# Kernel tuning notes

Hardware: AMD Instinct MI355X
Metric: run time of the kernel (lower is better)

## Reference

```python
import jax, jax.numpy as jnp
from jax import lax
import numpy as np

VOCAB, EMB = 50000, 300
HID, NCLS = 100, 20
BATCH, SEQ = 128, 512
P_DROP = 0.5


def setup_inputs() -> dict:
    key = jax.random.key(0)
    ks = jax.random.split(key, 8)
    s_e = 1.0 / np.sqrt(EMB)
    s_h = 1.0 / np.sqrt(HID)
    return {
        "inputs_batch": jax.random.randint(ks[0], (BATCH, SEQ), 0, VOCAB, dtype=jnp.int64)
        if jax.config.jax_enable_x64 else jax.random.randint(ks[0], (BATCH, SEQ), 0, VOCAB, dtype=jnp.int32),
        "emb_table": jax.random.normal(ks[1], (VOCAB, EMB), dtype=jnp.float32),
        # GRUCell params (torch layout): gates order [r, z, n]
        "w_ih": jax.random.uniform(ks[2], (3 * HID, EMB), jnp.float32, -s_h, s_h),
        "w_hh": jax.random.uniform(ks[3], (3 * HID, HID), jnp.float32, -s_h, s_h),
        "b_ih": jax.random.uniform(ks[4], (3 * HID,), jnp.float32, -s_h, s_h),
        "b_hh": jax.random.uniform(ks[5], (3 * HID,), jnp.float32, -s_h, s_h),
        "w_lin": jax.random.uniform(ks[6], (NCLS, HID), jnp.float32, -s_h, s_h),
        "b_lin": jax.random.uniform(ks[7], (NCLS,), jnp.float32, -s_h, s_h),
    }


def reference(inputs_batch, emb_table, w_ih, w_hh, b_ih, b_hh, w_lin, b_lin):
    B, S = inputs_batch.shape
    H = w_hh.shape[1]
    keep = 1.0 - P_DROP
    dk1, dk2 = jax.random.split(jax.random.key(42))

    z_embed = emb_table[inputs_batch]                       # [B, S, E]
    m1 = jax.random.bernoulli(dk1, keep, z_embed.shape)     # dropout1 mask
    z_embed = jnp.where(m1, z_embed / keep, 0.0)
    x_seq = jnp.swapaxes(z_embed, 0, 1)                     # [S, B, E]
    m2 = jax.random.bernoulli(dk2, keep, (S, B, H))         # per-step dropout2 masks

    def step(h, inp):
        x, m = inp
        gi = x @ w_ih.T + b_ih                              # [B, 3H]
        gh = h @ w_hh.T + b_hh
        i_r, i_z, i_n = jnp.split(gi, 3, axis=-1)
        h_r, h_z, h_n = jnp.split(gh, 3, axis=-1)
        r = jax.nn.sigmoid(i_r + h_r)
        zg = jax.nn.sigmoid(i_z + h_z)
        n = jnp.tanh(i_n + r * h_n)
        h_new = (1.0 - zg) * n + zg * h
        h_d = jnp.where(m, h_new / keep, 0.0)
        y = jax.nn.log_softmax(h_d @ w_lin.T + b_lin, axis=1)  # [B, C]
        return h_new, y

    h0 = jnp.zeros((B, H), dtype=x_seq.dtype)
    _, ys = lax.scan(step, h0, (x_seq, m2))                 # ys: [S, B, C]
    return jnp.transpose(ys, (1, 2, 0))                     # [B, C, S]
```

## Files before the change

### kernel.cpp

```cpp
#include <hip/hip_runtime.h>
#include <hip/hip_bf16.h>
#include <cstdint>

#define BATCH 128
#define SEQ   512
#define EMB   300
#define HID   100
#define G3    300
#define NCLS  20
#define NROWS (SEQ * BATCH)

#define M1_WORDS 614400
#define M2_WORDS 204800

typedef __attribute__((ext_vector_type(4))) float f32x4;
typedef __attribute__((ext_vector_type(8))) short s16x8;
typedef __fp16 h16x2 __attribute__((ext_vector_type(2)));

__host__ __device__ __forceinline__ void threefry2x32(uint32_t k0, uint32_t k1,
                                                      uint32_t x0, uint32_t x1,
                                                      uint32_t* o0, uint32_t* o1) {
  uint32_t ks2 = k0 ^ k1 ^ 0x1BD11BDAu;
  x0 += k0; x1 += k1;
#define TFR(r) { x0 += x1; x1 = (x1 << (r)) | (x1 >> (32 - (r))); x1 ^= x0; }
  TFR(13) TFR(15) TFR(26) TFR(6)  x0 += k1;  x1 += ks2 + 1u;
  TFR(17) TFR(29) TFR(16) TFR(24) x0 += ks2; x1 += k0 + 2u;
  TFR(13) TFR(15) TFR(26) TFR(6)  x0 += k0;  x1 += k1 + 3u;
  TFR(17) TFR(29) TFR(16) TFR(24) x0 += k1;  x1 += ks2 + 4u;
  TFR(13) TFR(15) TFR(26) TFR(6)  x0 += ks2; x1 += k0 + 5u;
#undef TFR
  *o0 = x0; *o1 = x1;
}

__device__ __forceinline__ uint32_t rand_bits32(uint32_t ka, uint32_t kb, uint32_t flat) {
  uint32_t a, b;
  threefry2x32(ka, kb, 0u, flat, &a, &b);
  return a ^ b;
}

__device__ __forceinline__ short f2bf(float f) {
  union { float f; uint32_t u; } c; c.f = f;
  uint32_t u = c.u;
  return (short)((u + 0x7FFFu + ((u >> 16) & 1u)) >> 16);
}

__device__ __forceinline__ void bar_lds() {
  __asm__ __volatile__("s_waitcnt lgkmcnt(0)" ::: "memory");
  __builtin_amdgcn_s_barrier();
  __asm__ __volatile__("" ::: "memory");
}

__device__ __forceinline__ float swz_xor4(float x) {
  return __builtin_bit_cast(float,
      __builtin_amdgcn_ds_swizzle(__builtin_bit_cast(int, x), 0x101F));
}

__global__ __launch_bounds__(256) void k_mask(uint32_t* __restrict__ M1w,
                                              uint32_t* __restrict__ M2w,
                                              uint32_t k1a, uint32_t k1b,
                                              uint32_t k2a, uint32_t k2b) {
  const int i = blockIdx.x * 256 + threadIdx.x;
  uint32_t ka, kb, base;
  uint32_t* dst;
  if (i < M1_WORDS) { ka = k1a; kb = k1b; base = (uint32_t)i * 32u; dst = M1w + i; }
  else { ka = k2a; kb = k2b; base = (uint32_t)(i - M1_WORDS) * 32u; dst = M2w + (i - M1_WORDS); }
  uint32_t w = 0u;
#pragma unroll
  for (int j = 0; j < 32; ++j) {
    uint32_t bits = rand_bits32(ka, kb, base + (uint32_t)j);
    w |= ((~bits) >> 31) << j;
  }
  *dst = w;
}

__global__ __launch_bounds__(256) void k_prepw(const float* __restrict__ w_ih,
                                               short* __restrict__ Wb) {
  int i8 = (blockIdx.x * 256 + threadIdx.x) * 8;
  if (i8 >= 304 * 320) return;
  short o[8];
#pragma unroll
  for (int j = 0; j < 8; ++j) {
    int pos = i8 + j;
    int n = pos / 320, k = pos - (pos / 320) * 320;
    float v = (n < 300 && k < 300) ? w_ih[(size_t)n * EMB + k] : 0.f;
    o[j] = f2bf(v);
  }
  *(s16x8*)(Wb + i8) = *(s16x8*)o;
}

__global__ __launch_bounds__(256) void k_prepx(const int* __restrict__ inputs,
                                               const float* __restrict__ emb,
                                               const uint32_t* __restrict__ M1w,
                                               short* __restrict__ Xb) {
  const int i8 = blockIdx.x * 256 + threadIdx.x;
  const int r = i8 / 40, c8 = i8 - r * 40;
  const int e = c8 * 8;
  const int b = r & 127, sq = r >> 7;
  short o[8];
  if (e >= 300) {
#pragma unroll
    for (int j = 0; j < 8; ++j) o[j] = 0;
  } else {
    const int tok = inputs[b * SEQ + sq];
    const float* er = emb + (size_t)tok * EMB + e;
    float xa[8];
    if (e + 8 <= 300) {
      float4 v0 = *(const float4*)(er);
      float4 v1 = *(const float4*)(er + 4);
      xa[0] = v0.x; xa[1] = v0.y; xa[2] = v0.z; xa[3] = v0.w;
      xa[4] = v1.x; xa[5] = v1.y; xa[6] = v1.z; xa[7] = v1.w;
    } else {
      float4 v0 = *(const float4*)(er);
      xa[0] = v0.x; xa[1] = v0.y; xa[2] = v0.z; xa[3] = v0.w;
      xa[4] = xa[5] = xa[6] = xa[7] = 0.f;
    }
    const uint32_t flat = (uint32_t)((b * SEQ + sq) * EMB + e);
    uint64_t mw = (uint64_t)M1w[flat >> 5] | ((uint64_t)M1w[(flat >> 5) + 1] << 32);
    uint32_t mb = (uint32_t)(mw >> (flat & 31));
#pragma unroll
    for (int j = 0; j < 8; ++j)
      o[j] = f2bf(((mb >> j) & 1u) ? xa[j] * 2.f : 0.f);
  }
  *(s16x8*)(Xb + (size_t)i8 * 8) = *(s16x8*)o;
}

__global__ __launch_bounds__(512) void k_gi8(const short* __restrict__ Xb,
                                             const short* __restrict__ Wb,
                                             const float* __restrict__ b_ih,
                                             float* __restrict__ GI) {
  __shared__ short As[128 * 40];
  __shared__ short Bs[304 * 40];
  const int t = threadIdx.x;
  const int s = blockIdx.x;
  const int lane = t & 63, wave = t >> 6;
  const int wr = wave & 1;
  const int wc = wave >> 1;
  const int ml = lane & 15, quad = lane >> 4;
  const int arow = t >> 2;
  const int akq = t & 3;

  const int nfr = (wc < 3) ? 5 : 4;
  f32x4 acc[4][5];
#pragma unroll
  for (int i = 0; i < 4; ++i)
#pragma unroll
    for (int j = 0; j < 5; ++j) acc[i][j] = (f32x4){0.f, 0.f, 0.f, 0.f};

  const short* xrow = Xb + ((size_t)(s * 128) + arow) * 320;

  for (int c = 0; c < 10; ++c) {
    s16x8 av = *(const s16x8*)(xrow + c * 32 + akq * 8);
    s16x8 bv0, bv1, bv2;
    {
      int i0 = t;
      bv0 = *(const s16x8*)(Wb + (size_t)(i0 >> 2) * 320 + c * 32 + (i0 & 3) * 8);
      int i1 = t + 512;
      bv1 = *(const s16x8*)(Wb + (size_t)(i1 >> 2) * 320 + c * 32 + (i1 & 3) * 8);
      if (t < 192) {
        int i2 = t + 1024;
        bv2 = *(const s16x8*)(Wb + (size_t)(i2 >> 2) * 320 + c * 32 + (i2 & 3) * 8);
      }
    }
    if (c > 0) __syncthreads();
    *(s16x8*)&As[arow * 40 + akq * 8] = av;
    {
      int i0 = t;       *(s16x8*)&Bs[(i0 >> 2) * 40 + (i0 & 3) * 8] = bv0;
      int i1 = t + 512; *(s16x8*)&Bs[(i1 >> 2) * 40 + (i1 & 3) * 8] = bv1;
      if (t < 192) { int i2 = t + 1024; *(s16x8*)&Bs[(i2 >> 2) * 40 + (i2 & 3) * 8] = bv2; }
    }
    __syncthreads();
    s16x8 af[4];
#pragma unroll
    for (int mt = 0; mt < 4; ++mt)
      af[mt] = *(const s16x8*)&As[(wr * 64 + mt * 16 + ml) * 40 + quad * 8];
#pragma unroll
    for (int j = 0; j < 5; ++j) {
      if (j < nfr) {
        int nt = wc + 4 * j;
        s16x8 bf = *(const s16x8*)&Bs[(nt * 16 + ml) * 40 + quad * 8];
#pragma unroll
        for (int mt = 0; mt < 4; ++mt)
          acc[mt][j] = __builtin_amdgcn_mfma_f32_16x16x32_bf16(af[mt], bf, acc[mt][j], 0, 0, 0);
      }
    }
  }

#pragma unroll
  for (int j = 0; j < 5; ++j) {
    if (j < nfr) {
      int n = (wc + 4 * j) * 16 + ml;
      if (n < 300) {
        float bias = b_ih[n];
#pragma unroll
        for (int mt = 0; mt < 4; ++mt) {
#pragma unroll
          for (int i = 0; i < 4; ++i) {
            int brow = wr * 64 + mt * 16 + quad * 4 + i;
            GI[(size_t)(s * BATCH + brow) * G3 + n] = acc[mt][j][i] + bias;
          }
        }
      }
    }
  }
}

__global__ __launch_bounds__(512) void k_gi7(const int* __restrict__ inputs,
                                             const float* __restrict__ emb,
                                             const short* __restrict__ Wb,
                                             const float* __restrict__ b_ih,
                                             const uint32_t* __restrict__ M1w,
                                             float* __restrict__ GI) {
  __shared__ short As[128 * 40];
  __shared__ short Bs[304 * 40];
  __shared__ int idxs[128];
  const int t = threadIdx.x;
  const int s = blockIdx.x;
  const int lane = t & 63, wave = t >> 6;
  const int wr = wave & 1;
  const int wc = wave >> 1;
  const int ml = lane & 15, quad = lane >> 4;
  const int arow = t >> 2;
  const int akq = t & 3;

  if (t < 128) idxs[t] = inputs[t * SEQ + s];
  __syncthreads();

  const int nfr = (wc < 3) ? 5 : 4;
  f32x4 acc[4][5];
#pragma unroll
  for (int i = 0; i < 4; ++i)
#pragma unroll
    for (int j = 0; j < 5; ++j) acc[i][j] = (f32x4){0.f, 0.f, 0.f, 0.f};

  const int myidx = idxs[arow];

  for (int c = 0; c < 10; ++c) {
    const int e0 = c * 32 + akq * 8;
    float xa[8];
#pragma unroll
    for (int j = 0; j < 8; ++j) xa[j] = 0.f;
    if (e0 + 7 < 300) {
#pragma unroll
      for (int q4 = 0; q4 < 2; ++q4) {
        float4 v = *(const float4*)(emb + (size_t)myidx * EMB + e0 + q4 * 4);
        xa[q4 * 4 + 0] = v.x; xa[q4 * 4 + 1] = v.y; xa[q4 * 4 + 2] = v.z; xa[q4 * 4 + 3] = v.w;
      }
    } else if (e0 < 300) {
#pragma unroll
      for (int j = 0; j < 8; ++j) {
        int e = e0 + j;
        if (e < 300) xa[j] = emb[(size_t)myidx * EMB + e];
      }
    }
    uint32_t mb = 0;
    if (e0 < 300) {
      uint32_t base = (uint32_t)((arow * SEQ + s) * EMB + e0);
      uint64_t mw = (uint64_t)M1w[base >> 5] | ((uint64_t)M1w[(base >> 5) + 1] << 32);
      mb = (uint32_t)(mw >> (base & 31));
    }
    short sa[8];
#pragma unroll
    for (int j = 0; j < 8; ++j)
      sa[j] = f2bf(((mb >> j) & 1u) ? xa[j] * 2.f : 0.f);
    s16x8 bv0, bv1, bv2;
    {
      int i0 = t;
      bv0 = *(const s16x8*)(Wb + (size_t)(i0 >> 2) * 320 + c * 32 + (i0 & 3) * 8);
      int i1 = t + 512;
      bv1 = *(const s16x8*)(Wb + (size_t)(i1 >> 2) * 320 + c * 32 + (i1 & 3) * 8);
      if (t < 192) {
        int i2 = t + 1024;
        bv2 = *(const s16x8*)(Wb + (size_t)(i2 >> 2) * 320 + c * 32 + (i2 & 3) * 8);
      }
    }
    if (c > 0) __syncthreads();
    *(s16x8*)&As[arow * 40 + akq * 8] = *(s16x8*)&sa[0];
    {
      int i0 = t;       *(s16x8*)&Bs[(i0 >> 2) * 40 + (i0 & 3) * 8] = bv0;
      int i1 = t + 512; *(s16x8*)&Bs[(i1 >> 2) * 40 + (i1 & 3) * 8] = bv1;
      if (t < 192) { int i2 = t + 1024; *(s16x8*)&Bs[(i2 >> 2) * 40 + (i2 & 3) * 8] = bv2; }
    }
    __syncthreads();
    s16x8 af[4];
#pragma unroll
    for (int mt = 0; mt < 4; ++mt)
      af[mt] = *(const s16x8*)&As[(wr * 64 + mt * 16 + ml) * 40 + quad * 8];
#pragma unroll
    for (int j = 0; j < 5; ++j) {
      if (j < nfr) {
        int nt = wc + 4 * j;
        s16x8 bf = *(const s16x8*)&Bs[(nt * 16 + ml) * 40 + quad * 8];
#pragma unroll
        for (int mt = 0; mt < 4; ++mt)
          acc[mt][j] = __builtin_amdgcn_mfma_f32_16x16x32_bf16(af[mt], bf, acc[mt][j], 0, 0, 0);
      }
    }
  }

#pragma unroll
  for (int j = 0; j < 5; ++j) {
    if (j < nfr) {
      int n = (wc + 4 * j) * 16 + ml;
      if (n < 300) {
        float bias = b_ih[n];
#pragma unroll
        for (int mt = 0; mt < 4; ++mt) {
#pragma unroll
          for (int i = 0; i < 4; ++i) {
            int brow = wr * 64 + mt * 16 + quad * 4 + i;
            GI[(size_t)(s * BATCH + brow) * G3 + n] = acc[mt][j][i] + bias;
          }
        }
      }
    }
  }
}

__global__ __launch_bounds__(512, 1) void k_rnn11(const float* __restrict__ GI,
                                                  const float* __restrict__ w_hh,
                                                  const float* __restrict__ b_hh,
                                                  const uint8_t* __restrict__ M2,
                                                  float* __restrict__ Hd) {
  __shared__ __align__(16) uint32_t hp_s[2][64];
  const int t = threadIdx.x, b = blockIdx.x;
  const int u = t >> 2, ks = t & 3;
  const bool act = (u < 100);
  const bool gate = act && (ks == 0);
  const int uc = act ? u : 99;
  const int kplo = (ks < 2) ? ks * 13 : 26 + (ks - 2) * 12;
  const int np = (ks < 2) ? 13 : 12;

  const float* rowR = w_hh + (size_t)uc * HID;
  const float* rowZ = w_hh + (size_t)(uc + 100) * HID;
  const float* rowN = w_hh + (size_t)(uc + 200) * HID;
  const h16x2 z2 = (h16x2){(__fp16)0.f, (__fp16)0.f};
  h16x2 wR[13], wZ[13], wN[13];
#pragma unroll
  for (int j = 0; j < 13; ++j) {
    if (j < np) {
      int o = 2 * (kplo + j);
      wR[j] = __builtin_amdgcn_cvt_pkrtz(rowR[o], rowR[o + 1]);
      wZ[j] = __builtin_amdgcn_cvt_pkrtz(rowZ[o], rowZ[o + 1]);
      wN[j] = __builtin_amdgcn_cvt_pkrtz(rowN[o], rowN[o + 1]);
    } else { wR[j] = z2; wZ[j] = z2; wN[j] = z2; }
  }

  float bR0 = 0.f, bZ0 = 0.f, bN0 = 0.f;
  float gcR = 0.f, gcZ = 0.f, gcN = 0.f;
  uint8_t mc = 0;
  if (gate) {
    bR0 = b_hh[u]; bZ0 = b_hh[100 + u]; bN0 = b_hh[200 + u];
    const float* g0 = GI + (size_t)b * G3;
    gcR = g0[u]; gcZ = g0[100 + u]; gcN = g0[200 + u];
    mc = M2[(uint32_t)(b * HID + u) >> 3];
  }
  const int p = u >> 1;
  const int sidx = (p < 13) ? 0 : (p < 26) ? 1 : (p < 38) ? 2 : 3;
  const int spos = p - ((sidx < 2) ? sidx * 13 : 26 + (sidx - 2) * 12);
  const int slot = sidx * 16 + spos;
  const bool writer = gate && !(u & 1);

  if (t < 128) ((uint32_t*)hp_s)[t] = 0u;
  float hprev = 0.f;
  __syncthreads();

#define QPX(x, c) __builtin_bit_cast(float, __builtin_amdgcn_mov_dpp( \
    __builtin_bit_cast(int, (x)), (c), 0xF, 0xF, true))
#define DOT1(J, W) { h16x2 hh = __builtin_bit_cast(h16x2, (W)); \
    sR = __builtin_amdgcn_fdot2(wR[J], hh, sR, false); \
    sZ = __builtin_amdgcn_fdot2(wZ[J], hh, sZ, false); \
    sN = __builtin_amdgcn_fdot2(wN[J], hh, sN, false); }

#pragma unroll 2
  for (int s = 0; s < SEQ; ++s) {
    float gnR = 0.f, gnZ = 0.f, gnN = 0.f;
    uint8_t mn = 0;
    if (gate) {
      int sn = (s + 1 < SEQ) ? s + 1 : s;
      const float* gp = GI + (size_t)(sn * BATCH + b) * G3;
      gnR = gp[u]; gnZ = gp[100 + u]; gnN = gp[200 + u];
      mn = M2[(uint32_t)((sn * BATCH + b) * HID + u) >> 3];
    }

    if (act) {
      float sR = bR0, sZ = bZ0, sN = bN0;
      const uint32_t* hb = &hp_s[s & 1][0] + (ks << 4);
      uint4 h0 = *(const uint4*)hb;
      uint4 h1 = *(const uint4*)(hb + 4);
      uint4 h2 = *(const uint4*)(hb + 8);
      uint32_t h3 = hb[12];
      DOT1(0, h0.x)  DOT1(1, h0.y)  DOT1(2, h0.z)  DOT1(3, h0.w)
      DOT1(4, h1.x)  DOT1(5, h1.y)  DOT1(6, h1.z)  DOT1(7, h1.w)
      DOT1(8, h2.x)  DOT1(9, h2.y)  DOT1(10, h2.z) DOT1(11, h2.w)
      DOT1(12, h3)
      sR += QPX(sR, 0xB1); sZ += QPX(sZ, 0xB1); sN += QPX(sN, 0xB1);
      sR += QPX(sR, 0x4E); sZ += QPX(sZ, 0x4E); sN += QPX(sN, 0x4E);
      if (gate) {
        float r = 1.f / (1.f + __expf(-(gcR + sR)));
        float z = 1.f / (1.f + __expf(-(gcZ + sZ)));
        float xn = gcN + r * sN;
        float e2 = __expf(2.f * fabsf(xn));
        float n = copysignf(1.f - 2.f / (e2 + 1.f), xn);
        float hnew = (1.f - z) * n + z * hprev;
        hprev = hnew;
        uint32_t fl = (uint32_t)((s * BATCH + b) * HID + u);
        float hd = ((mc >> (fl & 7)) & 1) ? hnew * 2.f : 0.f;
        Hd[(size_t)(b * SEQ + s) * HID + u] = hd;
        float hoth = swz_xor4(hnew);
        if (writer)
          hp_s[(s & 1) ^ 1][slot] =
              __builtin_bit_cast(uint32_t, __builtin_amdgcn_cvt_pkrtz(hnew, hoth));
      }
    }
    gcR = gnR; gcZ = gnZ; gcN = gnN; mc = mn;
    bar_lds();
  }
#undef DOT1
#undef QPX
}

__global__ __launch_bounds__(64) void k_out(const float* __restrict__ Hd,
                                            const float* __restrict__ w_lin,
                                            const float* __restrict__ b_lin,
                                            float* __restrict__ out) {
  __shared__ float Wl[NCLS * HID];
  __shared__ float bl[NCLS];
  const int t = threadIdx.x;
  for (int i = t; i < NCLS * HID; i += 64) Wl[i] = w_lin[i];
  if (t < NCLS) bl[t] = b_lin[t];
  __syncthreads();

  const int r0 = (blockIdx.x * 64 + t) * 4;
  float acc[4][NCLS];
#pragma unroll
  for (int r = 0; r < 4; ++r)
#pragma unroll
    for (int c = 0; c < NCLS; ++c) acc[r][c] = bl[c];

  for (int k = 0; k < HID; k += 4) {
    float4 h0 = *(const float4*)(Hd + (size_t)(r0 + 0) * HID + k);
    float4 h1 = *(const float4*)(Hd + (size_t)(r0 + 1) * HID + k);
    float4 h2 = *(const float4*)(Hd + (size_t)(r0 + 2) * HID + k);
    float4 h3 = *(const float4*)(Hd + (size_t)(r0 + 3) * HID + k);
#pragma unroll
    for (int c = 0; c < NCLS; ++c) {
      float4 w4 = *(const float4*)&Wl[c * HID + k];
      acc[0][c] += h0.x * w4.x + h0.y * w4.y + h0.z * w4.z + h0.w * w4.w;
      acc[1][c] += h1.x * w4.x + h1.y * w4.y + h1.z * w4.z + h1.w * w4.w;
      acc[2][c] += h2.x * w4.x + h2.y * w4.y + h2.z * w4.z + h2.w * w4.w;
      acc[3][c] += h3.x * w4.x + h3.y * w4.y + h3.z * w4.z + h3.w * w4.w;
    }
  }

  float lse[4];
#pragma unroll
  for (int r = 0; r < 4; ++r) {
    float mx = acc[r][0];
#pragma unroll
    for (int c = 1; c < NCLS; ++c) mx = fmaxf(mx, acc[r][c]);
    float se = 0.f;
#pragma unroll
    for (int c = 0; c < NCLS; ++c) se += __expf(acc[r][c] - mx);
    lse[r] = mx + __logf(se);
  }
  const int b = r0 >> 9, s0 = r0 & 511;
#pragma unroll
  for (int c = 0; c < NCLS; ++c) {
    float4 o = make_float4(acc[0][c] - lse[0], acc[1][c] - lse[1],
                           acc[2][c] - lse[2], acc[3][c] - lse[3]);
    *(float4*)(out + (size_t)(b * NCLS + c) * SEQ + s0) = o;
  }
}

extern "C" void kernel_launch(void* const* d_in, const int* in_sizes, int n_in,
                              void* d_out, int out_size, void* d_ws, size_t ws_size,
                              hipStream_t stream) {
  const int*   inputs = (const int*)d_in[0];
  const float* emb    = (const float*)d_in[1];
  const float* w_ih   = (const float*)d_in[2];
  const float* w_hh   = (const float*)d_in[3];
  const float* b_ih   = (const float*)d_in[4];
  const float* b_hh   = (const float*)d_in[5];
  const float* w_lin  = (const float*)d_in[6];
  const float* b_lin  = (const float*)d_in[7];
  float* out = (float*)d_out;

  float* GI = (float*)d_ws;
  float* Hd = GI + (size_t)NROWS * G3;
  uint8_t* M1 = (uint8_t*)(Hd + (size_t)NROWS * HID);
  uint8_t* M2 = M1 + (size_t)M1_WORDS * 4;
  short* Wb = (short*)(M2 + (size_t)M2_WORDS * 4);
  short* Xb = Wb + 304 * 320;
  const size_t need_xb = 150272000;

  uint32_t dk1a, dk1b, dk2a, dk2b;
  threefry2x32(0u, 42u, 0u, 0u, &dk1a, &dk1b);
  threefry2x32(0u, 42u, 0u, 1u, &dk2a, &dk2b);

  k_mask<<<(M1_WORDS + M2_WORDS) / 256, 256, 0, stream>>>(
      (uint32_t*)M1, (uint32_t*)M2, dk1a, dk1b, dk2a, dk2b);
  k_prepw<<<(304 * 320 / 8 + 255) / 256, 256, 0, stream>>>(w_ih, Wb);
  if (ws_size >= need_xb) {
    k_prepx<<<65536 * 40 / 256, 256, 0, stream>>>(inputs, emb,
                                                  (const uint32_t*)M1, Xb);
    k_gi8<<<512, 512, 0, stream>>>(Xb, Wb, b_ih, GI);
  } else {
    k_gi7<<<512, 512, 0, stream>>>(inputs, emb, Wb, b_ih, (const uint32_t*)M1, GI);
  }
  k_rnn11<<<BATCH, 512, 0, stream>>>(GI, w_hh, b_hh, M2, Hd);
  k_out<<<256, 64, 0, stream>>>(Hd, w_lin, b_lin, out);
}
```

Baseline: 559.4 us.

## Fuse all stages into one cooperative persistent kernel with grid syncs

Replaces the chain of mask, weight prep, input prep, GEMM, recurrence and output kernels with a single cooperative kernel of 256 blocks that separates the stages with grid-wide syncs. The embedding gather is fused into the GEMM A-tile load, so the bf16 Xb staging buffer is dropped. The output kernel now runs with one thread per row across the whole grid. The aim is to remove launch gaps and the round trip through Xb; in exchange, only 256 blocks do the GEMM and mask work, and the recurrence stage leaves half the blocks idle. If the cooperative launch fails, the old multi-kernel path runs instead.

```diff
diff --git a/kernel.cpp b/kernel.cpp
--- a/kernel.cpp
+++ b/kernel.cpp
@@ -1,6 +1,9 @@
 #include <hip/hip_runtime.h>
+#include <hip/hip_cooperative_groups.h>
 #include <hip/hip_bf16.h>
 #include <cstdint>
+
+namespace cg = cooperative_groups;
 
 #define BATCH 128
 #define SEQ   512
@@ -55,6 +58,297 @@
       __builtin_amdgcn_ds_swizzle(__builtin_bit_cast(int, x), 0x101F));
 }
 
+__global__ __launch_bounds__(512, 4) void k_all(
+    const int* __restrict__ inputs, const float* __restrict__ emb,
+    const float* __restrict__ w_ih, const float* __restrict__ w_hh,
+    const float* __restrict__ b_ih, const float* __restrict__ b_hh,
+    const float* __restrict__ w_lin, const float* __restrict__ b_lin,
+    float* __restrict__ out, float* __restrict__ GI, float* __restrict__ Hd,
+    uint32_t* __restrict__ M1w, uint32_t* __restrict__ M2w,
+    short* __restrict__ Wb,
+    uint32_t k1a, uint32_t k1b, uint32_t k2a, uint32_t k2b) {
+  __shared__ __align__(16) char smem[35072];
+  const int t = threadIdx.x, bid = blockIdx.x;
+  const int flat = bid * 512 + t;
+
+  for (int i = flat; i < M1_WORDS + M2_WORDS; i += 256 * 512) {
+    uint32_t ka, kb, base;
+    uint32_t* dst;
+    if (i < M1_WORDS) { ka = k1a; kb = k1b; base = (uint32_t)i * 32u; dst = M1w + i; }
+    else { ka = k2a; kb = k2b; base = (uint32_t)(i - M1_WORDS) * 32u; dst = M2w + (i - M1_WORDS); }
+    uint32_t w = 0u;
+#pragma unroll
+    for (int j = 0; j < 32; ++j) {
+      uint32_t bits = rand_bits32(ka, kb, base + (uint32_t)j);
+      w |= ((~bits) >> 31) << j;
+    }
+    *dst = w;
+  }
+  if (flat < 304 * 320 / 8) {
+    const int i8 = flat * 8;
+    short o[8];
+#pragma unroll
+    for (int j = 0; j < 8; ++j) {
+      int pos = i8 + j;
+      int n = pos / 320, k = pos - (pos / 320) * 320;
+      float v = (n < 300 && k < 300) ? w_ih[(size_t)n * EMB + k] : 0.f;
+      o[j] = f2bf(v);
+    }
+    *(s16x8*)(Wb + i8) = *(s16x8*)o;
+  }
+  __threadfence();
+  cg::this_grid().sync();
+  __threadfence();
+
+  {
+    short* As = (short*)smem;
+    short* Bs = As + 128 * 40;
+    int* idxs = (int*)(Bs + 304 * 40);
+    const int lane = t & 63, wave = t >> 6;
+    const int wr = wave & 1, wc = wave >> 1;
+    const int ml = lane & 15, quad = lane >> 4;
+    const int arow = t >> 2, akq = t & 3;
+    const int nfr = (wc < 3) ? 5 : 4;
+
+    for (int si = 0; si < 2; ++si) {
+      const int s = bid * 2 + si;
+      __syncthreads();
+      if (t < 128) idxs[t] = inputs[t * SEQ + s];
+      __syncthreads();
+
+      f32x4 acc[4][5];
+#pragma unroll
+      for (int i = 0; i < 4; ++i)
+#pragma unroll
+        for (int j = 0; j < 5; ++j) acc[i][j] = (f32x4){0.f, 0.f, 0.f, 0.f};
+
+      const int myidx = idxs[arow];
+
+      for (int c = 0; c < 10; ++c) {
+        const int e0 = c * 32 + akq * 8;
+        float xa[8];
+#pragma unroll
+        for (int j = 0; j < 8; ++j) xa[j] = 0.f;
+        if (e0 + 7 < 300) {
+#pragma unroll
+          for (int q4 = 0; q4 < 2; ++q4) {
+            float4 v = *(const float4*)(emb + (size_t)myidx * EMB + e0 + q4 * 4);
+            xa[q4 * 4 + 0] = v.x; xa[q4 * 4 + 1] = v.y;
+            xa[q4 * 4 + 2] = v.z; xa[q4 * 4 + 3] = v.w;
+          }
+        } else if (e0 < 300) {
+#pragma unroll
+          for (int j = 0; j < 8; ++j) {
+            int e = e0 + j;
+            if (e < 300) xa[j] = emb[(size_t)myidx * EMB + e];
+          }
+        }
+        uint32_t mb = 0;
+        if (e0 < 300) {
+          uint32_t base = (uint32_t)((arow * SEQ + s) * EMB + e0);
+          uint64_t mw = (uint64_t)M1w[base >> 5] | ((uint64_t)M1w[(base >> 5) + 1] << 32);
+          mb = (uint32_t)(mw >> (base & 31));
+        }
+        short sa[8];
+#pragma unroll
+        for (int j = 0; j < 8; ++j)
+          sa[j] = f2bf(((mb >> j) & 1u) ? xa[j] * 2.f : 0.f);
+        s16x8 bv0, bv1, bv2;
+        {
+          int i0 = t;
+          bv0 = *(const s16x8*)(Wb + (size_t)(i0 >> 2) * 320 + c * 32 + (i0 & 3) * 8);
+          int i1 = t + 512;
+          bv1 = *(const s16x8*)(Wb + (size_t)(i1 >> 2) * 320 + c * 32 + (i1 & 3) * 8);
+          if (t < 192) {
+            int i2 = t + 1024;
+            bv2 = *(const s16x8*)(Wb + (size_t)(i2 >> 2) * 320 + c * 32 + (i2 & 3) * 8);
+          }
+        }
+        if (c > 0) __syncthreads();
+        *(s16x8*)&As[arow * 40 + akq * 8] = *(s16x8*)&sa[0];
+        {
+          int i0 = t;       *(s16x8*)&Bs[(i0 >> 2) * 40 + (i0 & 3) * 8] = bv0;
+          int i1 = t + 512; *(s16x8*)&Bs[(i1 >> 2) * 40 + (i1 & 3) * 8] = bv1;
+          if (t < 192) { int i2 = t + 1024; *(s16x8*)&Bs[(i2 >> 2) * 40 + (i2 & 3) * 8] = bv2; }
+        }
+        __syncthreads();
+        s16x8 af[4];
+#pragma unroll
+        for (int mt = 0; mt < 4; ++mt)
+          af[mt] = *(const s16x8*)&As[(wr * 64 + mt * 16 + ml) * 40 + quad * 8];
+#pragma unroll
+        for (int j = 0; j < 5; ++j) {
+          if (j < nfr) {
+            int nt = wc + 4 * j;
+            s16x8 bf = *(const s16x8*)&Bs[(nt * 16 + ml) * 40 + quad * 8];
+#pragma unroll
+            for (int mt = 0; mt < 4; ++mt)
+              acc[mt][j] = __builtin_amdgcn_mfma_f32_16x16x32_bf16(af[mt], bf, acc[mt][j], 0, 0, 0);
+          }
+        }
+      }
+
+#pragma unroll
+      for (int j = 0; j < 5; ++j) {
+        if (j < nfr) {
+          int n = (wc + 4 * j) * 16 + ml;
+          if (n < 300) {
+            float bias = b_ih[n];
+#pragma unroll
+            for (int mt = 0; mt < 4; ++mt) {
+#pragma unroll
+              for (int i = 0; i < 4; ++i) {
+                int brow = wr * 64 + mt * 16 + quad * 4 + i;
+                GI[(size_t)(s * BATCH + brow) * G3 + n] = acc[mt][j][i] + bias;
+              }
+            }
+          }
+        }
+      }
+    }
+  }
+  __threadfence();
+  cg::this_grid().sync();
+  __threadfence();
+
+  if (bid < BATCH) {
+    uint32_t (*hp_s)[64] = (uint32_t (*)[64])smem;
+    const int b = bid;
+    const int u = t >> 2, ks = t & 3;
+    const bool act = (u < 100);
+    const bool gate = act && (ks == 0);
+    const int uc = act ? u : 99;
+    const int kplo = (ks < 2) ? ks * 13 : 26 + (ks - 2) * 12;
+    const int np = (ks < 2) ? 13 : 12;
+
+    const float* rowR = w_hh + (size_t)uc * HID;
+    const float* rowZ = w_hh + (size_t)(uc + 100) * HID;
+    const float* rowN = w_hh + (size_t)(uc + 200) * HID;
+    const h16x2 z2 = (h16x2){(__fp16)0.f, (__fp16)0.f};
+    h16x2 wR[13], wZ[13], wN[13];
+#pragma unroll
+    for (int j = 0; j < 13; ++j) {
+      if (j < np) {
+        int o = 2 * (kplo + j);
+        wR[j] = __builtin_amdgcn_cvt_pkrtz(rowR[o], rowR[o + 1]);
+        wZ[j] = __builtin_amdgcn_cvt_pkrtz(rowZ[o], rowZ[o + 1]);
+        wN[j] = __builtin_amdgcn_cvt_pkrtz(rowN[o], rowN[o + 1]);
+      } else { wR[j] = z2; wZ[j] = z2; wN[j] = z2; }
+    }
+
+    float bR0 = 0.f, bZ0 = 0.f, bN0 = 0.f;
+    float gcR = 0.f, gcZ = 0.f, gcN = 0.f;
+    uint8_t mc = 0;
+    const uint8_t* M2 = (const uint8_t*)M2w;
+    if (gate) {
+      bR0 = b_hh[u]; bZ0 = b_hh[100 + u]; bN0 = b_hh[200 + u];
+      const float* g0 = GI + (size_t)b * G3;
+      gcR = g0[u]; gcZ = g0[100 + u]; gcN = g0[200 + u];
+      mc = M2[(uint32_t)(b * HID + u) >> 3];
+    }
+    const int p = u >> 1;
+    const int sidx = (p < 13) ? 0 : (p < 26) ? 1 : (p < 38) ? 2 : 3;
+    const int spos = p - ((sidx < 2) ? sidx * 13 : 26 + (sidx - 2) * 12);
+    const int slot = sidx * 16 + spos;
+    const bool writer = gate && !(u & 1);
+
+    if (t < 128) ((uint32_t*)hp_s)[t] = 0u;
+    float hprev = 0.f;
+    __syncthreads();
+
+#define QPX(x, c) __builtin_bit_cast(float, __builtin_amdgcn_mov_dpp( \
+    __builtin_bit_cast(int, (x)), (c), 0xF, 0xF, true))
+#define DOT1(J, W) { h16x2 hh = __builtin_bit_cast(h16x2, (W)); \
+    sR = __builtin_amdgcn_fdot2(wR[J], hh, sR, false); \
+    sZ = __builtin_amdgcn_fdot2(wZ[J], hh, sZ, false); \
+    sN = __builtin_amdgcn_fdot2(wN[J], hh, sN, false); }
+
+#pragma unroll 2
+    for (int s = 0; s < SEQ; ++s) {
+      float gnR = 0.f, gnZ = 0.f, gnN = 0.f;
+      uint8_t mn = 0;
+      if (gate) {
+        int sn = (s + 1 < SEQ) ? s + 1 : s;
+        const float* gp = GI + (size_t)(sn * BATCH + b) * G3;
+        gnR = gp[u]; gnZ = gp[100 + u]; gnN = gp[200 + u];
+        mn = M2[(uint32_t)((sn * BATCH + b) * HID + u) >> 3];
+      }
+
+      if (act) {
+        float sR = bR0, sZ = bZ0, sN = bN0;
+        const uint32_t* hb = &hp_s[s & 1][0] + (ks << 4);
+        uint4 h0 = *(const uint4*)hb;
+        uint4 h1 = *(const uint4*)(hb + 4);
+        uint4 h2 = *(const uint4*)(hb + 8);
+        uint32_t h3 = hb[12];
+        DOT1(0, h0.x)  DOT1(1, h0.y)  DOT1(2, h0.z)  DOT1(3, h0.w)
+        DOT1(4, h1.x)  DOT1(5, h1.y)  DOT1(6, h1.z)  DOT1(7, h1.w)
+        DOT1(8, h2.x)  DOT1(9, h2.y)  DOT1(10, h2.z) DOT1(11, h2.w)
+        DOT1(12, h3)
+        sR += QPX(sR, 0xB1); sZ += QPX(sZ, 0xB1); sN += QPX(sN, 0xB1);
+        sR += QPX(sR, 0x4E); sZ += QPX(sZ, 0x4E); sN += QPX(sN, 0x4E);
+        if (gate) {
+          float r = 1.f / (1.f + __expf(-(gcR + sR)));
+          float z = 1.f / (1.f + __expf(-(gcZ + sZ)));
+          float xn = gcN + r * sN;
+          float e2 = __expf(2.f * fabsf(xn));
+          float n = copysignf(1.f - 2.f / (e2 + 1.f), xn);
+          float hnew = (1.f - z) * n + z * hprev;
+          hprev = hnew;
+          uint32_t fl = (uint32_t)((s * BATCH + b) * HID + u);
+          float hd = ((mc >> (fl & 7)) & 1) ? hnew * 2.f : 0.f;
+          Hd[(size_t)(b * SEQ + s) * HID + u] = hd;
+          float hoth = swz_xor4(hnew);
+          if (writer)
+            hp_s[(s & 1) ^ 1][slot] =
+                __builtin_bit_cast(uint32_t, __builtin_amdgcn_cvt_pkrtz(hnew, hoth));
+        }
+      }
+      gcR = gnR; gcZ = gnZ; gcN = gnN; mc = mn;
+      bar_lds();
+    }
+#undef DOT1
+#undef QPX
+  }
+  __threadfence();
+  cg::this_grid().sync();
+  __threadfence();
+
+  {
+    float* Wl = (float*)smem;
+    float* bl = Wl + NCLS * HID;
+    __syncthreads();
+    for (int i = t; i < NCLS * HID; i += 512) Wl[i] = w_lin[i];
+    if (t < NCLS) bl[t] = b_lin[t];
+    __syncthreads();
+    if (flat < NROWS) {
+      const int r = flat, b = r >> 9, s0 = r & 511;
+      const float* hrow = Hd + (size_t)r * HID;
+      float acc[NCLS];
+#pragma unroll
+      for (int c = 0; c < NCLS; ++c) acc[c] = bl[c];
+      for (int k = 0; k < HID; k += 4) {
+        const float4 h = *(const float4*)(hrow + k);
+#pragma unroll
+        for (int c = 0; c < NCLS; ++c) {
+          const float4 w4 = *(const float4*)&Wl[c * HID + k];
+          acc[c] += h.x * w4.x + h.y * w4.y + h.z * w4.z + h.w * w4.w;
+        }
+      }
+      float mx = acc[0];
+#pragma unroll
+      for (int c = 1; c < NCLS; ++c) mx = fmaxf(mx, acc[c]);
+      float se = 0.f;
+#pragma unroll
+      for (int c = 0; c < NCLS; ++c) se += __expf(acc[c] - mx);
+      const float lse = mx + __logf(se);
+#pragma unroll
+      for (int c = 0; c < NCLS; ++c)
+        out[(size_t)(b * NCLS + c) * SEQ + s0] = acc[c] - lse;
+    }
+  }
+}
+
 __global__ __launch_bounds__(256) void k_mask(uint32_t* __restrict__ M1w,
                                               uint32_t* __restrict__ M2w,
                                               uint32_t k1a, uint32_t k1b,
@@ -86,122 +380,6 @@
     o[j] = f2bf(v);
   }
   *(s16x8*)(Wb + i8) = *(s16x8*)o;
-}
-
-__global__ __launch_bounds__(256) void k_prepx(const int* __restrict__ inputs,
-                                               const float* __restrict__ emb,
-                                               const uint32_t* __restrict__ M1w,
-                                               short* __restrict__ Xb) {
-  const int i8 = blockIdx.x * 256 + threadIdx.x;
-  const int r = i8 / 40, c8 = i8 - r * 40;
-  const int e = c8 * 8;
-  const int b = r & 127, sq = r >> 7;
-  short o[8];
-  if (e >= 300) {
-#pragma unroll
-    for (int j = 0; j < 8; ++j) o[j] = 0;
-  } else {
-    const int tok = inputs[b * SEQ + sq];
-    const float* er = emb + (size_t)tok * EMB + e;
-    float xa[8];
-    if (e + 8 <= 300) {
-      float4 v0 = *(const float4*)(er);
-      float4 v1 = *(const float4*)(er + 4);
-      xa[0] = v0.x; xa[1] = v0.y; xa[2] = v0.z; xa[3] = v0.w;
-      xa[4] = v1.x; xa[5] = v1.y; xa[6] = v1.z; xa[7] = v1.w;
-    } else {
-      float4 v0 = *(const float4*)(er);
-      xa[0] = v0.x; xa[1] = v0.y; xa[2] = v0.z; xa[3] = v0.w;
-      xa[4] = xa[5] = xa[6] = xa[7] = 0.f;
-    }
-    const uint32_t flat = (uint32_t)((b * SEQ + sq) * EMB + e);
-    uint64_t mw = (uint64_t)M1w[flat >> 5] | ((uint64_t)M1w[(flat >> 5) + 1] << 32);
-    uint32_t mb = (uint32_t)(mw >> (flat & 31));
-#pragma unroll
-    for (int j = 0; j < 8; ++j)
-      o[j] = f2bf(((mb >> j) & 1u) ? xa[j] * 2.f : 0.f);
-  }
-  *(s16x8*)(Xb + (size_t)i8 * 8) = *(s16x8*)o;
-}
-
-__global__ __launch_bounds__(512) void k_gi8(const short* __restrict__ Xb,
-                                             const short* __restrict__ Wb,
-                                             const float* __restrict__ b_ih,
-                                             float* __restrict__ GI) {
-  __shared__ short As[128 * 40];
-  __shared__ short Bs[304 * 40];
-  const int t = threadIdx.x;
-  const int s = blockIdx.x;
-  const int lane = t & 63, wave = t >> 6;
-  const int wr = wave & 1;
-  const int wc = wave >> 1;
-  const int ml = lane & 15, quad = lane >> 4;
-  const int arow = t >> 2;
-  const int akq = t & 3;
-
-  const int nfr = (wc < 3) ? 5 : 4;
-  f32x4 acc[4][5];
-#pragma unroll
-  for (int i = 0; i < 4; ++i)
-#pragma unroll
-    for (int j = 0; j < 5; ++j) acc[i][j] = (f32x4){0.f, 0.f, 0.f, 0.f};
-
-  const short* xrow = Xb + ((size_t)(s * 128) + arow) * 320;
-
-  for (int c = 0; c < 10; ++c) {
-    s16x8 av = *(const s16x8*)(xrow + c * 32 + akq * 8);
-    s16x8 bv0, bv1, bv2;
-    {
-      int i0 = t;
-      bv0 = *(const s16x8*)(Wb + (size_t)(i0 >> 2) * 320 + c * 32 + (i0 & 3) * 8);
-      int i1 = t + 512;
-      bv1 = *(const s16x8*)(Wb + (size_t)(i1 >> 2) * 320 + c * 32 + (i1 & 3) * 8);
-      if (t < 192) {
-        int i2 = t + 1024;
-        bv2 = *(const s16x8*)(Wb + (size_t)(i2 >> 2) * 320 + c * 32 + (i2 & 3) * 8);
-      }
-    }
-    if (c > 0) __syncthreads();
-    *(s16x8*)&As[arow * 40 + akq * 8] = av;
-    {
-      int i0 = t;       *(s16x8*)&Bs[(i0 >> 2) * 40 + (i0 & 3) * 8] = bv0;
-      int i1 = t + 512; *(s16x8*)&Bs[(i1 >> 2) * 40 + (i1 & 3) * 8] = bv1;
-      if (t < 192) { int i2 = t + 1024; *(s16x8*)&Bs[(i2 >> 2) * 40 + (i2 & 3) * 8] = bv2; }
-    }
-    __syncthreads();
-    s16x8 af[4];
-#pragma unroll
-    for (int mt = 0; mt < 4; ++mt)
-      af[mt] = *(const s16x8*)&As[(wr * 64 + mt * 16 + ml) * 40 + quad * 8];
-#pragma unroll
-    for (int j = 0; j < 5; ++j) {
-      if (j < nfr) {
-        int nt = wc + 4 * j;
-        s16x8 bf = *(const s16x8*)&Bs[(nt * 16 + ml) * 40 + quad * 8];
-#pragma unroll
-        for (int mt = 0; mt < 4; ++mt)
-          acc[mt][j] = __builtin_amdgcn_mfma_f32_16x16x32_bf16(af[mt], bf, acc[mt][j], 0, 0, 0);
-      }
-    }
-  }
-
-#pragma unroll
-  for (int j = 0; j < 5; ++j) {
-    if (j < nfr) {
-      int n = (wc + 4 * j) * 16 + ml;
-      if (n < 300) {
-        float bias = b_ih[n];
-#pragma unroll
-        for (int mt = 0; mt < 4; ++mt) {
-#pragma unroll
-          for (int i = 0; i < 4; ++i) {
-            int brow = wr * 64 + mt * 16 + quad * 4 + i;
-            GI[(size_t)(s * BATCH + brow) * G3 + n] = acc[mt][j][i] + bias;
-          }
-        }
-      }
-    }
-  }
 }
 
 __global__ __launch_bounds__(512) void k_gi7(const int* __restrict__ inputs,
@@ -490,23 +668,28 @@
   uint8_t* M1 = (uint8_t*)(Hd + (size_t)NROWS * HID);
   uint8_t* M2 = M1 + (size_t)M1_WORDS * 4;
   short* Wb = (short*)(M2 + (size_t)M2_WORDS * 4);
-  short* Xb = Wb + 304 * 320;
-  const size_t need_xb = 150272000;
 
   uint32_t dk1a, dk1b, dk2a, dk2b;
   threefry2x32(0u, 42u, 0u, 0u, &dk1a, &dk1b);
   threefry2x32(0u, 42u, 0u, 1u, &dk2a, &dk2b);
 
-  k_mask<<<(M1_WORDS + M2_WORDS) / 256, 256, 0, stream>>>(
-      (uint32_t*)M1, (uint32_t*)M2, dk1a, dk1b, dk2a, dk2b);
-  k_prepw<<<(304 * 320 / 8 + 255) / 256, 256, 0, stream>>>(w_ih, Wb);
-  if (ws_size >= need_xb) {
-    k_prepx<<<65536 * 40 / 256, 256, 0, stream>>>(inputs, emb,
-                                                  (const uint32_t*)M1, Xb);
-    k_gi8<<<512, 512, 0, stream>>>(Xb, Wb, b_ih, GI);
-  } else {
-    k_gi7<<<512, 512, 0, stream>>>(inputs, emb, Wb, b_ih, (const uint32_t*)M1, GI);
-  }
-  k_rnn11<<<BATCH, 512, 0, stream>>>(GI, w_hh, b_hh, M2, Hd);
-  k_out<<<256, 64, 0, stream>>>(Hd, w_lin, b_lin, out);
-}
+  uint32_t* M1u = (uint32_t*)M1;
+  uint32_t* M2u = (uint32_t*)M2;
+  void* kargs[] = {
+      (void*)&inputs, (void*)&emb, (void*)&w_ih, (void*)&w_hh,
+      (void*)&b_ih, (void*)&b_hh, (void*)&w_lin, (void*)&b_lin,
+      (void*)&out, (void*)&GI, (void*)&Hd, (void*)&M1u, (void*)&M2u,
+      (void*)&Wb, (void*)&dk1a, (void*)&dk1b, (void*)&dk2a, (void*)&dk2b };
+
+  hipError_t err = hipLaunchCooperativeKernel((const void*)k_all, dim3(256),
+                                              dim3(512), kargs, 0, stream);
+  if (err != hipSuccess) {
+    (void)hipGetLastError();
+    k_mask<<<(M1_WORDS + M2_WORDS) / 256, 256, 0, stream>>>(
+        M1u, M2u, dk1a, dk1b, dk2a, dk2b);
+    k_prepw<<<(304 * 320 / 8 + 255) / 256, 256, 0, stream>>>(w_ih, Wb);
+    k_gi7<<<512, 512, 0, stream>>>(inputs, emb, Wb, b_ih, M1u, GI);
+    k_rnn11<<<BATCH, 512, 0, stream>>>(GI, w_hh, b_hh, M2, Hd);
+    k_out<<<256, 64, 0, stream>>>(Hd, w_lin, b_lin, out);
+  }
+}
```

New measurement: 938.9 us. 1.68x slower.
